# Performance work log

Measured on AMD Instinct MI355X. Metric: run time of the kernel, lower is better.

Reference implementation:

```python
import jax, jax.numpy as jnp
import numpy as np

N = 50000        # num_nodes
E = 1_600_000    # num_edges (before self loops)
IN = 128         # in_channels
C = 16           # out_channels per head
H = 4            # heads
ED = 16          # edge_dim
SLOPE = 0.2      # LeakyReLU negative slope


def setup_inputs() -> dict:
    key = jax.random.key(0)
    ks = jax.random.split(key, 9)
    x = jax.random.normal(ks[0], (N, IN), jnp.float32)
    edge_index = jax.random.randint(ks[1], (2, E), 0, N)
    edge_attr = jax.random.normal(ks[2], (E, ED), jnp.float32)
    # GATConv parameters (PyG layout): node lin (no bias), attention vectors, edge lin
    W = jax.random.normal(ks[3], (IN, H * C), jnp.float32) / np.float32(np.sqrt(IN))
    att_src = jax.random.normal(ks[4], (H, C), jnp.float32) / np.float32(np.sqrt(C))
    att_dst = jax.random.normal(ks[5], (H, C), jnp.float32) / np.float32(np.sqrt(C))
    W_edge = jax.random.normal(ks[6], (ED, H * C), jnp.float32) / np.float32(np.sqrt(ED))
    att_edge = jax.random.normal(ks[7], (H, C), jnp.float32) / np.float32(np.sqrt(C))
    bias = jnp.zeros((H * C,), jnp.float32)
    return {"x": x, "edge_index": edge_index, "edge_attr": edge_attr,
            "W": W, "att_src": att_src, "att_dst": att_dst,
            "W_edge": W_edge, "att_edge": att_edge, "bias": bias}


def reference(x, edge_index, edge_attr, W, att_src, att_dst, W_edge, att_edge, bias):
    num_nodes = x.shape[0]
    # GATLayer: add self loops (PyG fills self-loop edge_attr with 1.0)
    loops = jnp.arange(num_nodes, dtype=edge_index.dtype)
    ei = jnp.concatenate([edge_index, jnp.stack([loops, loops])], axis=1)
    ea = jnp.concatenate(
        [edge_attr, jnp.ones((num_nodes, edge_attr.shape[1]), edge_attr.dtype)], axis=0)
    src, dst = ei[0], ei[1]  # messages flow src -> dst
    # eval mode: feat_dropout / edge_dropout are no-ops
    h = (x @ W).reshape(num_nodes, H, C)              # [N,H,C]
    a_src = jnp.einsum('nhc,hc->nh', h, att_src)       # [N,H]
    a_dst = jnp.einsum('nhc,hc->nh', h, att_dst)       # [N,H]
    e = (ea @ W_edge).reshape(-1, H, C)                # [E',H,C]
    a_e = jnp.einsum('ehc,hc->eh', e, att_edge)        # [E',H]
    alpha = a_src[src] + a_dst[dst] + a_e              # per-edge logits [E',H]
    alpha = jax.nn.leaky_relu(alpha, SLOPE)
    # segment softmax over incoming edges of each dst node (every node has a self loop)
    amax = jax.ops.segment_max(alpha, dst, num_segments=num_nodes)
    ex = jnp.exp(alpha - amax[dst])
    denom = jax.ops.segment_sum(ex, dst, num_segments=num_nodes)
    att = ex / denom[dst]                              # [E',H]
    # scatter-add aggregation of weighted source features
    out = jax.ops.segment_sum(att[:, :, None] * h[src], dst, num_segments=num_nodes)
    return out.reshape(num_nodes, H * C) + bias        # concat heads + bias
```

## Files before the change

### kernel.cpp

```cpp
#include <hip/hip_runtime.h>
#include <hip/hip_bf16.h>
#include <cstdint>

#define IN_CH 128
#define HC    64
#define ED    16
#define SLOPE 0.2f

typedef float        f32x4 __attribute__((ext_vector_type(4)));
typedef unsigned int u32x4 __attribute__((ext_vector_type(4)));

__device__ __forceinline__ uint32_t f2bf(float x) {
  uint32_t b = __float_as_uint(x);
  return (b + 0x7fffu + ((b >> 16) & 1u)) >> 16;
}
__device__ __forceinline__ float bf2f(uint32_t h) {
  return __uint_as_float(h << 16);
}

__global__ __launch_bounds__(256) void k_node(
    const float* __restrict__ x, const float* __restrict__ W,
    const float* __restrict__ att_src_p, const float* __restrict__ att_dst_p,
    uint16_t* __restrict__ hb, float* __restrict__ a_src, float* __restrict__ a_dst,
    int N)
{
  int lane = threadIdx.x & 63;
  int gw = (blockIdx.x * blockDim.x + threadIdx.x) >> 6;
  int nwaves = (gridDim.x * blockDim.x) >> 6;
  float asv = att_src_p[lane];
  float adv = att_dst_p[lane];
  for (int n0 = gw * 4; n0 < N; n0 += nwaves * 4) {
    int n1 = min(n0 + 1, N - 1), n2 = min(n0 + 2, N - 1), n3 = min(n0 + 3, N - 1);
    const f32x4* xa = (const f32x4*)(x + (size_t)n0 * IN_CH);
    const f32x4* xb = (const f32x4*)(x + (size_t)n1 * IN_CH);
    const f32x4* xc = (const f32x4*)(x + (size_t)n2 * IN_CH);
    const f32x4* xd = (const f32x4*)(x + (size_t)n3 * IN_CH);
    float acc0 = 0.f, acc1 = 0.f, acc2 = 0.f, acc3 = 0.f;
#pragma unroll 4
    for (int k4 = 0; k4 < IN_CH / 4; k4++) {
      f32x4 va = __builtin_nontemporal_load(xa + k4);
      f32x4 vb = __builtin_nontemporal_load(xb + k4);
      f32x4 vc = __builtin_nontemporal_load(xc + k4);
      f32x4 vd = __builtin_nontemporal_load(xd + k4);
      float w0 = W[(k4 * 4 + 0) * HC + lane];
      float w1 = W[(k4 * 4 + 1) * HC + lane];
      float w2 = W[(k4 * 4 + 2) * HC + lane];
      float w3 = W[(k4 * 4 + 3) * HC + lane];
      acc0 += va.x * w0 + va.y * w1 + va.z * w2 + va.w * w3;
      acc1 += vb.x * w0 + vb.y * w1 + vb.z * w2 + vb.w * w3;
      acc2 += vc.x * w0 + vc.y * w1 + vc.z * w2 + vc.w * w3;
      acc3 += vd.x * w0 + vd.y * w1 + vd.z * w2 + vd.w * w3;
    }
    hb[(size_t)n0 * HC + lane] = (uint16_t)f2bf(acc0);
    if (n0 + 1 < N) hb[(size_t)n1 * HC + lane] = (uint16_t)f2bf(acc1);
    if (n0 + 2 < N) hb[(size_t)n2 * HC + lane] = (uint16_t)f2bf(acc2);
    if (n0 + 3 < N) hb[(size_t)n3 * HC + lane] = (uint16_t)f2bf(acc3);
    float s0 = acc0 * asv, s1 = acc1 * asv, s2 = acc2 * asv, s3 = acc3 * asv;
    float d0 = acc0 * adv, d1 = acc1 * adv, d2 = acc2 * adv, d3 = acc3 * adv;
#pragma unroll
    for (int m = 1; m < 16; m <<= 1) {
      s0 += __shfl_xor(s0, m); s1 += __shfl_xor(s1, m);
      s2 += __shfl_xor(s2, m); s3 += __shfl_xor(s3, m);
      d0 += __shfl_xor(d0, m); d1 += __shfl_xor(d1, m);
      d2 += __shfl_xor(d2, m); d3 += __shfl_xor(d3, m);
    }
    if ((lane & 15) == 0) {
      int hh = lane >> 4;
      a_src[(size_t)n0 * 4 + hh] = s0; a_dst[(size_t)n0 * 4 + hh] = d0;
      if (n0 + 1 < N) { a_src[(size_t)n1 * 4 + hh] = s1; a_dst[(size_t)n1 * 4 + hh] = d1; }
      if (n0 + 2 < N) { a_src[(size_t)n2 * 4 + hh] = s2; a_dst[(size_t)n2 * 4 + hh] = d2; }
      if (n0 + 3 < N) { a_src[(size_t)n3 * 4 + hh] = s3; a_dst[(size_t)n3 * 4 + hh] = d3; }
    }
  }
}

__global__ __launch_bounds__(256) void k_hist(const int* __restrict__ dst, int E,
                                              int* __restrict__ deg)
{
  int e = blockIdx.x * 256 + threadIdx.x;
  if (e < E) atomicAdd(&deg[__builtin_nontemporal_load(dst + e)], 1);
}

__global__ __launch_bounds__(256) void k_scan_a(const int* __restrict__ deg, int N,
                                                int* __restrict__ rowptr,
                                                int* __restrict__ blksums)
{
  __shared__ int tsum[256];
  int tid = threadIdx.x;
  int base = blockIdx.x * 2048 + tid * 8;
  int pre[8];
  int s = 0;
#pragma unroll
  for (int j = 0; j < 8; j++) {
    int idx = base + j;
    int v = (idx < N) ? deg[idx] : 0;
    pre[j] = s; s += v;
  }
  tsum[tid] = s;
  __syncthreads();
  for (int offm = 1; offm < 256; offm <<= 1) {
    int t = (tid >= offm) ? tsum[tid - offm] : 0;
    __syncthreads();
    tsum[tid] += t;
    __syncthreads();
  }
  int excl = tsum[tid] - s;
#pragma unroll
  for (int j = 0; j < 8; j++) {
    int idx = base + j;
    if (idx < N) rowptr[idx] = excl + pre[j];
  }
  if (tid == 255) blksums[blockIdx.x] = tsum[255];
}

__global__ void k_scan_b(int* __restrict__ blksums, int NB)
{
  if (threadIdx.x == 0 && blockIdx.x == 0) {
    int run = 0;
    for (int b = 0; b < NB; b++) { int t = blksums[b]; blksums[b] = run; run += t; }
  }
}

__global__ __launch_bounds__(256) void k_scan_c(int* __restrict__ rowptr,
                                                int* __restrict__ cursor,
                                                const int* __restrict__ blksums,
                                                int N, int E)
{
  int i = blockIdx.x * 256 + threadIdx.x;
  if (i < N) {
    int v = rowptr[i] + blksums[i >> 11];
    rowptr[i] = v;
    cursor[i] = v;
  }
  if (i == 0) rowptr[N] = E;
}

__global__ __launch_bounds__(256) void k_edge5(
    const int* __restrict__ ei, const float* __restrict__ ea,
    const float* __restrict__ W_edge, const float* __restrict__ att_edge,
    const float* __restrict__ a_src, const float* __restrict__ a_dst,
    int* __restrict__ cursor, u32x4* __restrict__ pay, int E)
{
  __shared__ float ve[ED * 4];
  if (threadIdx.x < 64) {
    int d = threadIdx.x >> 2, hh = threadIdx.x & 3;
    float s = 0.f;
#pragma unroll
    for (int c = 0; c < 16; c++) s += W_edge[d * HC + hh * 16 + c] * att_edge[hh * 16 + c];
    ve[d * 4 + hh] = s;
  }
  __syncthreads();
  int e = blockIdx.x * 256 + threadIdx.x;
  if (e >= E) return;
  int sn = __builtin_nontemporal_load(ei + e);
  int dn = __builtin_nontemporal_load(ei + E + e);
  float4 as4 = *(const float4*)(a_src + (size_t)sn * 4);
  float4 ad4 = *(const float4*)(a_dst + (size_t)dn * 4);
  const f32x4* ea4 = (const f32x4*)(ea + (size_t)e * ED);
  f32x4 q0 = __builtin_nontemporal_load(ea4 + 0);
  f32x4 q1 = __builtin_nontemporal_load(ea4 + 1);
  f32x4 q2 = __builtin_nontemporal_load(ea4 + 2);
  f32x4 q3 = __builtin_nontemporal_load(ea4 + 3);
  float eav[16] = {q0.x,q0.y,q0.z,q0.w, q1.x,q1.y,q1.z,q1.w,
                   q2.x,q2.y,q2.z,q2.w, q3.x,q3.y,q3.z,q3.w};
  float ae0 = 0.f, ae1 = 0.f, ae2 = 0.f, ae3 = 0.f;
#pragma unroll
  for (int d = 0; d < ED; d++) {
    float v = eav[d];
    ae0 += v * ve[d * 4 + 0]; ae1 += v * ve[d * 4 + 1];
    ae2 += v * ve[d * 4 + 2]; ae3 += v * ve[d * 4 + 3];
  }
  float al0 = as4.x + ad4.x + ae0;
  float al1 = as4.y + ad4.y + ae1;
  float al2 = as4.z + ad4.z + ae2;
  float al3 = as4.w + ad4.w + ae3;
  al0 = al0 > 0.f ? al0 : SLOPE * al0;
  al1 = al1 > 0.f ? al1 : SLOPE * al1;
  al2 = al2 > 0.f ? al2 : SLOPE * al2;
  al3 = al3 > 0.f ? al3 : SLOPE * al3;
  int pos = atomicAdd(&cursor[dn], 1);
  u32x4 r;
  r.x = (uint32_t)sn * (HC * 2);
  r.y = f2bf(__expf(al0)) | (f2bf(__expf(al1)) << 16);
  r.z = f2bf(__expf(al2)) | (f2bf(__expf(al3)) << 16);
  r.w = 0u;
  pay[pos] = r;
}

__global__ __launch_bounds__(256) void k_agg5(
    const uint16_t* __restrict__ hb,
    const float* __restrict__ a_src, const float* __restrict__ a_dst,
    const float* __restrict__ W_edge, const float* __restrict__ att_edge,
    const float* __restrict__ bias, const int* __restrict__ rowptr,
    const u32x4* __restrict__ pay, float* __restrict__ out, int N)
{
  __shared__ float aes[4];
  if (threadIdx.x < 4) {
    int hh = threadIdx.x;
    float s = 0.f;
    for (int d = 0; d < ED; d++) {
      float vd = 0.f;
#pragma unroll
      for (int c = 0; c < 16; c++) vd += W_edge[d * HC + hh * 16 + c] * att_edge[hh * 16 + c];
      s += vd;
    }
    aes[hh] = s;
  }
  __syncthreads();
  int lane = threadIdx.x & 63;
  int n = blockIdx.x * 4 + (threadIdx.x >> 6);
  if (n >= N) return;
  int hq = lane >> 4;
  bool selz = (hq & 2) != 0;
  bool selh = (hq & 1) != 0;
  uint32_t lane2 = (uint32_t)lane * 2;
  const uint8_t* hbb = (const uint8_t*)hb;
  int b = rowptr[n], e = rowptr[n + 1];
  float acc = 0.f, den = 0.f;
  int p = b;
  for (; p + 7 < e; p += 8) {
    u32x4 r[8];
#pragma unroll
    for (int j = 0; j < 8; j++) r[j] = pay[p + j];
    float ee[8];
    uint32_t off[8];
#pragma unroll
    for (int j = 0; j < 8; j++) {
      uint32_t w = selz ? r[j].z : r[j].y;
      ee[j] = __uint_as_float(selh ? (w & 0xffff0000u) : (w << 16));
      off[j] = r[j].x + lane2;
    }
    float hv[8];
#pragma unroll
    for (int j = 0; j < 8; j++)
      hv[j] = bf2f(*(const uint16_t*)(hbb + off[j]));
#pragma unroll
    for (int j = 0; j < 8; j++) { acc += ee[j] * hv[j]; den += ee[j]; }
  }
  for (; p < e; p++) {
    u32x4 r0 = pay[p];
    uint32_t w = selz ? r0.z : r0.y;
    float e0 = __uint_as_float(selh ? (w & 0xffff0000u) : (w << 16));
    acc += e0 * bf2f(*(const uint16_t*)(hbb + r0.x + lane2));
    den += e0;
  }
  float al = a_src[(size_t)n * 4 + hq] + a_dst[(size_t)n * 4 + hq] + aes[hq];
  al = al > 0.f ? al : SLOPE * al;
  float exs = __expf(al);
  acc += exs * bf2f(*(const uint16_t*)(hbb + (uint32_t)n * (HC * 2) + lane2));
  den += exs;
  __builtin_nontemporal_store(acc / den + bias[lane], out + (size_t)n * HC + lane);
}

extern "C" void kernel_launch(void* const* d_in, const int* in_sizes, int n_in,
                              void* d_out, int out_size, void* d_ws, size_t ws_size,
                              hipStream_t stream)
{
  const float* x        = (const float*)d_in[0];
  const int*   ei       = (const int*)d_in[1];
  const float* ea       = (const float*)d_in[2];
  const float* W        = (const float*)d_in[3];
  const float* att_src  = (const float*)d_in[4];
  const float* att_dst  = (const float*)d_in[5];
  const float* W_edge   = (const float*)d_in[6];
  const float* att_edge = (const float*)d_in[7];
  const float* bias     = (const float*)d_in[8];
  float* out = (float*)d_out;

  int N = in_sizes[0] / IN_CH;
  int E = in_sizes[1] / 2;

  uint8_t* ws = (uint8_t*)d_ws;
  size_t off = 0;
  auto alloc = [&](size_t bytes) -> void* {
    void* p = ws + off;
    off = (off + bytes + 255) & ~(size_t)255;
    return p;
  };
  uint16_t* hb    = (uint16_t*)alloc((size_t)N * HC * 2);
  float* a_src_w  = (float*)alloc((size_t)N * 4 * 4);
  float* a_dst_w  = (float*)alloc((size_t)N * 4 * 4);
  int*   deg      = (int*)alloc((size_t)N * 4);
  int*   cursor   = (int*)alloc((size_t)N * 4);
  int*   rowptr   = (int*)alloc(((size_t)N + 1) * 4);
  int*   blksums  = (int*)alloc(64 * 4);
  u32x4* pay      = (u32x4*)alloc((size_t)E * 16);
  (void)ws_size; (void)n_in; (void)out_size;

  hipMemsetAsync(deg, 0, (size_t)N * 4, stream);

  k_node<<<512, 256, 0, stream>>>(x, W, att_src, att_dst, hb, a_src_w, a_dst_w, N);
  k_hist<<<(E + 255) / 256, 256, 0, stream>>>(ei + E, E, deg);
  int NB = (N + 2047) / 2048;
  k_scan_a<<<NB, 256, 0, stream>>>(deg, N, rowptr, blksums);
  k_scan_b<<<1, 64, 0, stream>>>(blksums, NB);
  k_scan_c<<<(N + 255) / 256, 256, 0, stream>>>(rowptr, cursor, blksums, N, E);
  k_edge5<<<(E + 255) / 256, 256, 0, stream>>>(ei, ea, W_edge, att_edge,
                                               a_src_w, a_dst_w, cursor, pay, E);
  k_agg5<<<(N + 3) / 4, 256, 0, stream>>>(hb, a_src_w, a_dst_w, W_edge, att_edge,
                                          bias, rowptr, pay, out, N);
}
```

Measured before the change: 510.0 us.

## Software-pipeline payload loads in aggregation, remap blocks across XCDs, nontemporal payload stores

The aggregation kernel now prefetches the next group of eight edge payloads while gathering features for the current group, hiding payload load latency behind the gather. Block indices are remapped so that each of the eight partitions gets a contiguous range of node blocks. This is meant to give each XCD's L2 a contiguous slice of the payload and row pointer data. The edge kernel writes its payload with nontemporal stores to reduce cache pollution, at the risk of losing L2 hits when the aggregation kernel reads the payload soon after. The prefetch raises register pressure.

```diff
diff --git a/kernel.cpp b/kernel.cpp
--- a/kernel.cpp
+++ b/kernel.cpp
@@ -135,7 +135,7 @@
   if (i == 0) rowptr[N] = E;
 }
 
-__global__ __launch_bounds__(256) void k_edge5(
+__global__ __launch_bounds__(256) void k_edge6(
     const int* __restrict__ ei, const float* __restrict__ ea,
     const float* __restrict__ W_edge, const float* __restrict__ att_edge,
     const float* __restrict__ a_src, const float* __restrict__ a_dst,
@@ -184,15 +184,16 @@
   r.y = f2bf(__expf(al0)) | (f2bf(__expf(al1)) << 16);
   r.z = f2bf(__expf(al2)) | (f2bf(__expf(al3)) << 16);
   r.w = 0u;
-  pay[pos] = r;
-}
-
-__global__ __launch_bounds__(256) void k_agg5(
+  __builtin_nontemporal_store(r, pay + pos);
+}
+
+__global__ __launch_bounds__(256) void k_agg6(
     const uint16_t* __restrict__ hb,
     const float* __restrict__ a_src, const float* __restrict__ a_dst,
     const float* __restrict__ W_edge, const float* __restrict__ att_edge,
     const float* __restrict__ bias, const int* __restrict__ rowptr,
-    const u32x4* __restrict__ pay, float* __restrict__ out, int N)
+    const u32x4* __restrict__ pay, float* __restrict__ out, int N,
+    int nb_per_part)
 {
   __shared__ float aes[4];
   if (threadIdx.x < 4) {
@@ -207,8 +208,11 @@
     aes[hh] = s;
   }
   __syncthreads();
+  int part = blockIdx.x & 7;
+  int bin = blockIdx.x >> 3;
+  int nblk = part * nb_per_part + bin;
   int lane = threadIdx.x & 63;
-  int n = blockIdx.x * 4 + (threadIdx.x >> 6);
+  int n = nblk * 4 + (threadIdx.x >> 6);
   if (n >= N) return;
   int hq = lane >> 4;
   bool selz = (hq & 2) != 0;
@@ -217,25 +221,39 @@
   const uint8_t* hbb = (const uint8_t*)hb;
   int b = rowptr[n], e = rowptr[n + 1];
   float acc = 0.f, den = 0.f;
+  int cnt8 = (e - b) & ~7;
+  int e8 = b + cnt8;
   int p = b;
-  for (; p + 7 < e; p += 8) {
+  if (p < e8) {
     u32x4 r[8];
 #pragma unroll
     for (int j = 0; j < 8; j++) r[j] = pay[p + j];
-    float ee[8];
-    uint32_t off[8];
-#pragma unroll
-    for (int j = 0; j < 8; j++) {
-      uint32_t w = selz ? r[j].z : r[j].y;
-      ee[j] = __uint_as_float(selh ? (w & 0xffff0000u) : (w << 16));
-      off[j] = r[j].x + lane2;
-    }
-    float hv[8];
-#pragma unroll
-    for (int j = 0; j < 8; j++)
-      hv[j] = bf2f(*(const uint16_t*)(hbb + off[j]));
-#pragma unroll
-    for (int j = 0; j < 8; j++) { acc += ee[j] * hv[j]; den += ee[j]; }
+    while (true) {
+      float ee[8];
+      uint32_t off[8];
+#pragma unroll
+      for (int j = 0; j < 8; j++) {
+        uint32_t w = selz ? r[j].z : r[j].y;
+        ee[j] = __uint_as_float(selh ? (w & 0xffff0000u) : (w << 16));
+        off[j] = r[j].x + lane2;
+      }
+      int pn = p + 8;
+      u32x4 rn[8];
+      if (pn < e8) {
+#pragma unroll
+        for (int j = 0; j < 8; j++) rn[j] = pay[pn + j];
+      }
+      float hv[8];
+#pragma unroll
+      for (int j = 0; j < 8; j++)
+        hv[j] = bf2f(*(const uint16_t*)(hbb + off[j]));
+#pragma unroll
+      for (int j = 0; j < 8; j++) { acc += ee[j] * hv[j]; den += ee[j]; }
+      p = pn;
+      if (p >= e8) break;
+#pragma unroll
+      for (int j = 0; j < 8; j++) r[j] = rn[j];
+    }
   }
   for (; p < e; p++) {
     u32x4 r0 = pay[p];
@@ -295,8 +313,10 @@
   k_scan_a<<<NB, 256, 0, stream>>>(deg, N, rowptr, blksums);
   k_scan_b<<<1, 64, 0, stream>>>(blksums, NB);
   k_scan_c<<<(N + 255) / 256, 256, 0, stream>>>(rowptr, cursor, blksums, N, E);
-  k_edge5<<<(E + 255) / 256, 256, 0, stream>>>(ei, ea, W_edge, att_edge,
+  k_edge6<<<(E + 255) / 256, 256, 0, stream>>>(ei, ea, W_edge, att_edge,
                                                a_src_w, a_dst_w, cursor, pay, E);
-  k_agg5<<<(N + 3) / 4, 256, 0, stream>>>(hb, a_src_w, a_dst_w, W_edge, att_edge,
-                                          bias, rowptr, pay, out, N);
-}
+  int nblocks = (N + 3) / 4;
+  int nb_per_part = (nblocks + 7) / 8;
+  k_agg6<<<nb_per_part * 8, 256, 0, stream>>>(hb, a_src_w, a_dst_w, W_edge, att_edge,
+                                              bias, rowptr, pay, out, N, nb_per_part);
+}
```

Result: slower. 641.5 us (+25.8%).

## Split edge scatter into sequential write plus group-partitioned binning pass

Applied to the files above, without the earlier changes.

The edge kernel now writes each edge's payload sequentially, with the destination node stored in the spare word, instead of doing an atomic cursor bump and a random scatter write. A new binning kernel splits destination nodes into 8 ranges. Each block group rescans all edges and scatters only those whose destination falls in its range, so atomics and writes stay within a smaller, more cache-local region. The cost is an extra E*16-byte intermediate buffer, one extra write of it, and eight re-reads of it.

```diff
diff --git a/kernel.cpp b/kernel.cpp
--- a/kernel.cpp
+++ b/kernel.cpp
@@ -135,11 +135,11 @@
   if (i == 0) rowptr[N] = E;
 }
 
-__global__ __launch_bounds__(256) void k_edge5(
+__global__ __launch_bounds__(256) void k_edge7(
     const int* __restrict__ ei, const float* __restrict__ ea,
     const float* __restrict__ W_edge, const float* __restrict__ att_edge,
     const float* __restrict__ a_src, const float* __restrict__ a_dst,
-    int* __restrict__ cursor, u32x4* __restrict__ pay, int E)
+    u32x4* __restrict__ seq, int E)
 {
   __shared__ float ve[ED * 4];
   if (threadIdx.x < 64) {
@@ -178,13 +178,31 @@
   al1 = al1 > 0.f ? al1 : SLOPE * al1;
   al2 = al2 > 0.f ? al2 : SLOPE * al2;
   al3 = al3 > 0.f ? al3 : SLOPE * al3;
-  int pos = atomicAdd(&cursor[dn], 1);
   u32x4 r;
   r.x = (uint32_t)sn * (HC * 2);
   r.y = f2bf(__expf(al0)) | (f2bf(__expf(al1)) << 16);
   r.z = f2bf(__expf(al2)) | (f2bf(__expf(al3)) << 16);
-  r.w = 0u;
-  pay[pos] = r;
+  r.w = (uint32_t)dn;
+  seq[e] = r;
+}
+
+__global__ __launch_bounds__(256) void k_bin(
+    const u32x4* __restrict__ seq, int* __restrict__ cursor,
+    u32x4* __restrict__ pay, int E, int N, int blocks_per_grp)
+{
+  int g = blockIdx.x & 7;
+  int sub = blockIdx.x >> 3;
+  uint32_t glo = (uint32_t)((size_t)N * g / 8);
+  uint32_t ghi = (uint32_t)((size_t)N * (g + 1) / 8);
+  int stride = blocks_per_grp * 256;
+  for (int e = sub * 256 + threadIdx.x; e < E; e += stride) {
+    u32x4 r = seq[e];
+    uint32_t dn = r.w;
+    if (dn >= glo && dn < ghi) {
+      int pos = atomicAdd(&cursor[dn], 1);
+      pay[pos] = r;
+    }
+  }
 }
 
 __global__ __launch_bounds__(256) void k_agg5(
@@ -284,6 +302,7 @@
   int*   cursor   = (int*)alloc((size_t)N * 4);
   int*   rowptr   = (int*)alloc(((size_t)N + 1) * 4);
   int*   blksums  = (int*)alloc(64 * 4);
+  u32x4* seq      = (u32x4*)alloc((size_t)E * 16);
   u32x4* pay      = (u32x4*)alloc((size_t)E * 16);
   (void)ws_size; (void)n_in; (void)out_size;
 
@@ -295,8 +314,10 @@
   k_scan_a<<<NB, 256, 0, stream>>>(deg, N, rowptr, blksums);
   k_scan_b<<<1, 64, 0, stream>>>(blksums, NB);
   k_scan_c<<<(N + 255) / 256, 256, 0, stream>>>(rowptr, cursor, blksums, N, E);
-  k_edge5<<<(E + 255) / 256, 256, 0, stream>>>(ei, ea, W_edge, att_edge,
-                                               a_src_w, a_dst_w, cursor, pay, E);
+  k_edge7<<<(E + 255) / 256, 256, 0, stream>>>(ei, ea, W_edge, att_edge,
+                                               a_src_w, a_dst_w, seq, E);
+  int blocks_per_grp = 256;
+  k_bin<<<blocks_per_grp * 8, 256, 0, stream>>>(seq, cursor, pay, E, N, blocks_per_grp);
   k_agg5<<<(N + 3) / 4, 256, 0, stream>>>(hb, a_src_w, a_dst_w, W_edge, att_edge,
                                           bias, rowptr, pay, out, N);
 }
```

After: 534.6 us. 1.05x slower.
